# Optimization experiments

Hardware: AMD Instinct MI355X
Metric: run time of the kernel (lower is better)

## Reference

```python
import jax, jax.numpy as jnp
import numpy as np

EPS = 1e-5  # nn.LayerNorm default
TOP_K = 2


def setup_inputs() -> dict:
    key = jax.random.key(0)
    ks = jax.random.split(key, 8)
    B, S, D, H, E = 4, 2048, 512, 512, 8
    sd = lambda fan_in: 1.0 / np.sqrt(fan_in)
    x = jax.random.normal(ks[0], (B, S, D), dtype=jnp.float32)
    # gate: Linear(D, E, bias=False)
    Wg = jax.random.uniform(ks[1], (D, E), jnp.float32, -sd(D), sd(D))
    # stacked expert params (ExpertModule): fc1 D->H, fc2 H->D, LayerNorm(D)
    W1 = jax.random.uniform(ks[2], (E, D, H), jnp.float32, -sd(D), sd(D))
    b1 = jax.random.uniform(ks[3], (E, H), jnp.float32, -sd(D), sd(D))
    W2 = jax.random.uniform(ks[4], (E, H, D), jnp.float32, -sd(H), sd(H))
    b2 = jax.random.uniform(ks[5], (E, D), jnp.float32, -sd(H), sd(H))
    gamma = jnp.ones((E, D), jnp.float32)
    beta = jnp.zeros((E, D), jnp.float32)
    return {"x": x, "Wg": Wg, "W1": W1, "b1": b1, "W2": W2, "b2": b2,
            "gamma": gamma, "beta": beta}


def _moe_forward(x, Wg, W1, b1, W2, b2, gamma, beta):
    B, S, D = x.shape
    xf = x.reshape(-1, D)                                   # [T, D]
    # gating: top-k logits then softmax over the k selected logits only
    logits = xf @ Wg                                        # [T, E]
    topv, topi = jax.lax.top_k(logits, TOP_K)               # [T, K]
    gate_w = jax.nn.softmax(topv, axis=-1)                  # [T, K]
    # expert MLP + LayerNorm computed for all experts (dropout inactive in eval)
    h = jax.nn.relu(jnp.einsum('td,edh->teh', xf, W1) + b1[None])   # [T, E, H]
    y = jnp.einsum('teh,ehd->ted', h, W2) + b2[None]                 # [T, E, D]
    mu = jnp.mean(y, axis=-1, keepdims=True)
    var = jnp.mean((y - mu) ** 2, axis=-1, keepdims=True)
    y = (y - mu) / jnp.sqrt(var + EPS) * gamma[None] + beta[None]
    # combine: gather the k selected expert outputs and weight-sum
    y_sel = jnp.take_along_axis(y, topi[:, :, None], axis=1)        # [T, K, D]
    out = jnp.sum(gate_w[:, :, None] * y_sel, axis=1)               # [T, D]
    return out.reshape(B, S, D)


def reference(x, Wg, W1, b1, W2, b2, gamma, beta):
    return _moe_forward(x, Wg, W1, b1, W2, b2, gamma, beta)
```

## Files before the change

kernel.cpp:

```cpp
#include <hip/hip_runtime.h>
#include <hip/hip_bf16.h>


#define T_TOK   8192
#define DDIM    512
#define HDIM    512
#define NEXP    8
#define NASSIGN (T_TOK * 2)
#define CPAD    16
#define CAP     4096
#define MT      40

typedef _Float16 f16x8 __attribute__((ext_vector_type(8)));
typedef _Float16 f16x4 __attribute__((ext_vector_type(4)));
typedef float    f32x4 __attribute__((ext_vector_type(4)));

__device__ __forceinline__ void gld_lds16(const _Float16* g, _Float16* l) {
    __builtin_amdgcn_global_load_lds(
        (const __attribute__((address_space(1))) unsigned int*)g,
        (__attribute__((address_space(3))) unsigned int*)l,
        16, 0, 0);
}

__global__ __launch_bounds__(256) void prep_kernel(
    const float* __restrict__ x,
    const float* __restrict__ Wg,
    const float* __restrict__ W1,
    const float* __restrict__ W2,
    _Float16* __restrict__ xh,
    int* __restrict__ ei,
    float* __restrict__ gw,
    int* __restrict__ cursor,
    int* __restrict__ rowtok,
    int* __restrict__ pos,
    _Float16* __restrict__ W1t,
    _Float16* __restrict__ W2t)
{
    __shared__ float wgt[NEXP][512];
    __shared__ float tile[32][33];
    __shared__ int lcnt[NEXP];
    __shared__ int gbase[NEXP];

    int bid = blockIdx.x;
    int tid = threadIdx.x;

    if (bid < 2048) {
        if (tid < NEXP) lcnt[tid] = 0;
#pragma unroll
        for (int r = 0; r < 2; r++) {
            int d = r * 256 + tid;
            const float4* wr = (const float4*)(Wg + (size_t)d * NEXP);
            float4 a = wr[0], b = wr[1];
            wgt[0][d] = a.x; wgt[1][d] = a.y; wgt[2][d] = a.z; wgt[3][d] = a.w;
            wgt[4][d] = b.x; wgt[5][d] = b.y; wgt[6][d] = b.z; wgt[7][d] = b.w;
        }
        __syncthreads();

        int lane = tid & 63;
        int wave = tid >> 6;
        int t = bid * 4 + wave;

        double acc[NEXP];
#pragma unroll
        for (int e = 0; e < NEXP; e++) acc[e] = 0.0;

#pragma unroll
        for (int jj = 0; jj < 2; jj++) {
            int d0 = jj * 256 + lane * 4;
            float4 xv = *(const float4*)(x + (size_t)t * DDIM + d0);
            f16x4 hv;
            hv[0] = (_Float16)xv.x; hv[1] = (_Float16)xv.y;
            hv[2] = (_Float16)xv.z; hv[3] = (_Float16)xv.w;
            *(f16x4*)(xh + (size_t)t * DDIM + d0) = hv;
            double xd[4] = {(double)xv.x, (double)xv.y, (double)xv.z, (double)xv.w};
#pragma unroll
            for (int e = 0; e < NEXP; e++) {
                f32x4 wv = *(const f32x4*)(&wgt[e][d0]);
#pragma unroll
                for (int c = 0; c < 4; c++)
                    acc[e] += xd[c] * (double)wv[c];
            }
        }
#pragma unroll
        for (int off = 1; off < 8; off <<= 1) {
#pragma unroll
            for (int e = 0; e < NEXP; e++) acc[e] += __shfl_xor(acc[e], off, 64);
        }
        double v = acc[0];
#pragma unroll
        for (int e = 1; e < NEXP; e++) if ((lane & 7) == e) v = acc[e];
#pragma unroll
        for (int off = 8; off < 64; off <<= 1) v += __shfl_xor(v, off, 64);
        double lv[NEXP];
#pragma unroll
        for (int e = 0; e < NEXP; e++) lv[e] = __shfl(v, e, 64);

        double v0 = -1e300; int i0 = 0;
#pragma unroll
        for (int e = 0; e < NEXP; e++) if (lv[e] > v0) { v0 = lv[e]; i0 = e; }
        double v1 = -1e300; int i1 = (i0 == 0) ? 1 : 0;
#pragma unroll
        for (int e = 0; e < NEXP; e++) if (e != i0 && lv[e] > v1) { v1 = lv[e]; i1 = e; }

        int lr0 = 0, lr1 = 0;
        if (lane == 0) {
            double ex = exp(v1 - v0);
            float g0 = (float)(1.0 / (1.0 + ex));
            float g1 = (float)(ex / (1.0 + ex));
            ei[2 * t] = i0;  ei[2 * t + 1] = i1;
            gw[2 * t] = g0;  gw[2 * t + 1] = g1;
            lr0 = atomicAdd(&lcnt[i0], 1);
            lr1 = atomicAdd(&lcnt[i1], 1);
        }
        __syncthreads();
        if (tid < NEXP) {
            int c = lcnt[tid];
            gbase[tid] = c ? atomicAdd(&cursor[tid * CPAD], c) : 0;
        }
        __syncthreads();
        if (lane == 0) {
            int r0 = i0 * CAP + gbase[i0] + lr0;
            int r1 = i1 * CAP + gbase[i1] + lr1;
            rowtok[r0] = 2 * t;      pos[2 * t] = r0;
            rowtok[r1] = 2 * t + 1;  pos[2 * t + 1] = r1;
        }
    } else {
        int b2 = bid - 2048;
        int z = b2 >> 8;
        int rem = b2 & 255;
        int by = (rem >> 4) * 32;
        int bx = (rem & 15) * 32;
        const float* src;
        _Float16* dst;
        if (z < 8) { src = W1 + (size_t)z * 512 * 512; dst = W1t + (size_t)z * 512 * 512; }
        else       { src = W2 + (size_t)(z - 8) * 512 * 512; dst = W2t + (size_t)(z - 8) * 512 * 512; }
        int tx = tid & 31, ty = tid >> 5;
#pragma unroll
        for (int i = 0; i < 4; i++) {
            int r = by + ty + i * 8;
            tile[ty + i * 8][tx] = src[(size_t)r * 512 + bx + tx];
        }
        __syncthreads();
        int row = tid >> 3;
        int jc  = tid & 7;
        f16x4 v;
#pragma unroll
        for (int k = 0; k < 4; k++) v[k] = (_Float16)tile[jc * 4 + k][row];
        *(f16x4*)(dst + (size_t)(bx + row) * 512 + by + jc * 4) = v;
    }
}

template <bool GATHER, bool RELU>
__global__ __launch_bounds__(256) void gemm_tile(
    const _Float16* __restrict__ A,
    const _Float16* __restrict__ Bt,
    const float* __restrict__ bias,
    const int* __restrict__ rowtok,
    const int* __restrict__ cursor,
    _Float16* __restrict__ C)
{
    int bid = blockIdx.x;
    int e = bid & 7;
    int j = bid >> 3;
    int ne = cursor[e * CPAD];
    int m0 = (j >> 2) * 64;
    if (m0 >= ne) return;
    int n0 = (j & 3) * 128;
    int off = e * CAP;
    const _Float16* Bte = Bt + (size_t)e * 512 * 512;

    __shared__ _Float16 As[2][64 * 32];
    __shared__ _Float16 Bs[2][128 * 32];

    int tid = threadIdx.x;
    int lane = tid & 63;
    int wave = tid >> 6;
    int wm = (wave >> 1) * 32;
    int wn = (wave & 1) * 64;
    int quad = lane >> 4;
    int l16 = lane & 15;

    int srow = tid >> 2;
    int ksw = ((tid & 3) ^ ((srow >> 1) & 3)) * 8;

    int rg0 = m0 + srow;
    int cr0 = off + (rg0 < ne ? rg0 : ne - 1);
    const _Float16* arow;
    if (GATHER) arow = A + (size_t)(rowtok[cr0] >> 1) * 512;
    else        arow = A + (size_t)cr0 * 512;
    const _Float16* brow0 = Bte + (size_t)(n0 + srow) * 512;
    const _Float16* brow1 = Bte + (size_t)(n0 + srow + 64) * 512;

    f32x4 acc[2][4];
#pragma unroll
    for (int i = 0; i < 2; i++)
#pragma unroll
        for (int jj = 0; jj < 4; jj++) {
            acc[i][jj][0] = 0.f; acc[i][jj][1] = 0.f;
            acc[i][jj][2] = 0.f; acc[i][jj][3] = 0.f;
        }

    int rsw = (quad ^ ((l16 >> 1) & 3)) * 8;

    gld_lds16(arow + ksw, &As[0][tid * 8]);
    gld_lds16(brow0 + ksw, &Bs[0][tid * 8]);
    gld_lds16(brow1 + ksw, &Bs[0][tid * 8 + 64 * 32]);
    __syncthreads();

    int cur = 0;
    for (int t = 0; t < 16; ++t) {
        if (t < 15) {
            int k1 = (t + 1) * 32;
            gld_lds16(arow + k1 + ksw, &As[cur ^ 1][tid * 8]);
            gld_lds16(brow0 + k1 + ksw, &Bs[cur ^ 1][tid * 8]);
            gld_lds16(brow1 + k1 + ksw, &Bs[cur ^ 1][tid * 8 + 64 * 32]);
        }

        f16x8 af[2], bf[4];
#pragma unroll
        for (int i = 0; i < 2; i++)
            af[i] = *(const f16x8*)(&As[cur][(wm + i * 16 + l16) * 32 + rsw]);
#pragma unroll
        for (int jj = 0; jj < 4; jj++)
            bf[jj] = *(const f16x8*)(&Bs[cur][(wn + jj * 16 + l16) * 32 + rsw]);
#pragma unroll
        for (int i = 0; i < 2; i++)
#pragma unroll
            for (int jj = 0; jj < 4; jj++)
                acc[i][jj] = __builtin_amdgcn_mfma_f32_16x16x32_f16(af[i], bf[jj], acc[i][jj], 0, 0, 0);

        if (t < 15) {
            __syncthreads();
            cur ^= 1;
        }
    }

    float bcol[4];
#pragma unroll
    for (int jj = 0; jj < 4; jj++) bcol[jj] = bias[(size_t)e * 512 + n0 + wn + jj * 16 + l16];
#pragma unroll
    for (int i = 0; i < 2; i++) {
#pragma unroll
        for (int rr = 0; rr < 4; rr++) {
            int rg = m0 + wm + i * 16 + quad * 4 + rr;
            if (rg < ne) {
#pragma unroll
                for (int jj = 0; jj < 4; jj++) {
                    float v = acc[i][jj][rr] + bcol[jj];
                    if (RELU) v = fmaxf(v, 0.0f);
                    C[(size_t)(off + rg) * 512 + n0 + wn + jj * 16 + l16] = (_Float16)v;
                }
            }
        }
    }
}

__global__ void ln_combine_kernel(const _Float16* __restrict__ yb,
                                  const int* __restrict__ pos,
                                  const float* __restrict__ gw,
                                  const int* __restrict__ ei,
                                  const float* __restrict__ gamma,
                                  const float* __restrict__ beta,
                                  float* __restrict__ out) {
    int t = blockIdx.x * 4 + (threadIdx.x >> 6);
    int lane = threadIdx.x & 63;
    float o[8];
#pragma unroll
    for (int j = 0; j < 8; j++) o[j] = 0.0f;

#pragma unroll
    for (int k = 0; k < 2; k++) {
        int s = 2 * t + k;
        int r = pos[s];
        int e = ei[s];
        float w = gw[s];
        f16x8 v = *(const f16x8*)(yb + (size_t)r * 512 + lane * 8);
        float f[8];
        float sum = 0.f, sq = 0.f;
#pragma unroll
        for (int j = 0; j < 8; j++) { f[j] = (float)v[j]; sum += f[j]; sq += f[j] * f[j]; }
#pragma unroll
        for (int off = 1; off < 64; off <<= 1) {
            sum += __shfl_xor(sum, off, 64);
            sq  += __shfl_xor(sq, off, 64);
        }
        float mu = sum * (1.0f / 512.0f);
        float var = sq * (1.0f / 512.0f) - mu * mu;
        float rstd = rsqrtf(var + 1e-5f);
#pragma unroll
        for (int j = 0; j < 8; j++) {
            int d = lane * 8 + j;
            o[j] += w * ((f[j] - mu) * rstd * gamma[(size_t)e * 512 + d] + beta[(size_t)e * 512 + d]);
        }
    }
    float4* op = (float4*)(out + (size_t)t * 512 + lane * 8);
    op[0] = make_float4(o[0], o[1], o[2], o[3]);
    op[1] = make_float4(o[4], o[5], o[6], o[7]);
}

extern "C" void kernel_launch(void* const* d_in, const int* in_sizes, int n_in,
                              void* d_out, int out_size, void* d_ws, size_t ws_size,
                              hipStream_t stream) {
    const float* x     = (const float*)d_in[0];
    const float* Wg    = (const float*)d_in[1];
    const float* W1    = (const float*)d_in[2];
    const float* b1    = (const float*)d_in[3];
    const float* W2    = (const float*)d_in[4];
    const float* b2    = (const float*)d_in[5];
    const float* gamma = (const float*)d_in[6];
    const float* beta  = (const float*)d_in[7];
    float* out = (float*)d_out;

    char* w = (char*)d_ws;
    size_t o = 0;
    auto alloc = [&](size_t bytes) -> void* {
        void* p = w + o;
        o += (bytes + 255) & ~(size_t)255;
        return p;
    };
    _Float16* xh  = (_Float16*)alloc((size_t)T_TOK * DDIM * 2);
    _Float16* W1t = (_Float16*)alloc((size_t)NEXP * DDIM * HDIM * 2);
    _Float16* W2t = (_Float16*)alloc((size_t)NEXP * DDIM * HDIM * 2);
    _Float16* hb  = (_Float16*)alloc((size_t)NEXP * CAP * HDIM * 2);
    _Float16* yb  = (_Float16*)alloc((size_t)NEXP * CAP * DDIM * 2);
    float* gw     = (float*)alloc((size_t)NASSIGN * 4);
    int* ei       = (int*)alloc((size_t)NASSIGN * 4);
    int* rowtok   = (int*)alloc((size_t)NEXP * CAP * 4);
    int* pos      = (int*)alloc((size_t)NASSIGN * 4);
    int* cursor   = (int*)alloc(NEXP * CPAD * 4);
    (void)ws_size; (void)n_in; (void)in_sizes; (void)out_size;

    hipMemsetAsync(cursor, 0, NEXP * CPAD * sizeof(int), stream);

    prep_kernel<<<6144, 256, 0, stream>>>(x, Wg, W1, W2, xh, ei, gw,
                                          cursor, rowtok, pos, W1t, W2t);

    gemm_tile<true, true><<<1280, 256, 0, stream>>>(xh, W1t, b1, rowtok, cursor, hb);
    gemm_tile<false, false><<<1280, 256, 0, stream>>>(hb, W2t, b2, nullptr, cursor, yb);

    ln_combine_kernel<<<2048, 256, 0, stream>>>(yb, pos, gw, ei, gamma, beta, out);
}
```

Before: 167.5 us.

## Enlarge prep blocks to 1024 threads, ballot-based expert slot allocation, vectorize combine loads

The prep kernel now uses 1024-thread blocks that handle 16 tokens (or four transpose tiles) each, which cuts the number of blocks and the redundant per-block loads of the gate weights. Slot allocation moves from shared-memory atomics plus two barriers to one wave doing ballot/popcount grouping with a single global atomic per expert. The x loads are issued before the gate-weight staging so they overlap. The combine kernel loads pos/ei/gw as vector pairs and gamma/beta as float4. Larger blocks may lower occupancy flexibility, and rows are now assigned within an expert in a different order.

```diff
diff --git a/kernel.cpp b/kernel.cpp
--- a/kernel.cpp
+++ b/kernel.cpp
@@ -22,7 +22,7 @@
         16, 0, 0);
 }
 
-__global__ __launch_bounds__(256) void prep_kernel(
+__global__ __launch_bounds__(1024) void prep_kernel(
     const float* __restrict__ x,
     const float* __restrict__ Wg,
     const float* __restrict__ W1,
@@ -36,42 +36,51 @@
     _Float16* __restrict__ W1t,
     _Float16* __restrict__ W2t)
 {
-    __shared__ float wgt[NEXP][512];
-    __shared__ float tile[32][33];
-    __shared__ int lcnt[NEXP];
-    __shared__ int gbase[NEXP];
+    __shared__ float smf[4 * 32 * 33];
+    __shared__ int earr[32];
 
     int bid = blockIdx.x;
     int tid = threadIdx.x;
 
-    if (bid < 2048) {
-        if (tid < NEXP) lcnt[tid] = 0;
-#pragma unroll
-        for (int r = 0; r < 2; r++) {
-            int d = r * 256 + tid;
-            const float4* wr = (const float4*)(Wg + (size_t)d * NEXP);
-            float4 a = wr[0], b = wr[1];
-            wgt[0][d] = a.x; wgt[1][d] = a.y; wgt[2][d] = a.z; wgt[3][d] = a.w;
-            wgt[4][d] = b.x; wgt[5][d] = b.y; wgt[6][d] = b.z; wgt[7][d] = b.w;
-        }
-        __syncthreads();
-
+    if (bid < 512) {
+        float (*wgt)[512] = (float (*)[512])smf;
         int lane = tid & 63;
         int wave = tid >> 6;
-        int t = bid * 4 + wave;
+        int t = bid * 16 + wave;
+
+        const float* xr = x + (size_t)t * DDIM;
+        float4 xv0 = *(const float4*)(xr + lane * 4);
+        float4 xv1 = *(const float4*)(xr + 256 + lane * 4);
+
+        if (tid < 256) {
+#pragma unroll
+            for (int r = 0; r < 2; r++) {
+                int d = r * 256 + tid;
+                const float4* wr = (const float4*)(Wg + (size_t)d * NEXP);
+                float4 a = wr[0], b = wr[1];
+                wgt[0][d] = a.x; wgt[1][d] = a.y; wgt[2][d] = a.z; wgt[3][d] = a.w;
+                wgt[4][d] = b.x; wgt[5][d] = b.y; wgt[6][d] = b.z; wgt[7][d] = b.w;
+            }
+        }
+
+        {
+            f16x4 h0, h1;
+            h0[0] = (_Float16)xv0.x; h0[1] = (_Float16)xv0.y;
+            h0[2] = (_Float16)xv0.z; h0[3] = (_Float16)xv0.w;
+            h1[0] = (_Float16)xv1.x; h1[1] = (_Float16)xv1.y;
+            h1[2] = (_Float16)xv1.z; h1[3] = (_Float16)xv1.w;
+            *(f16x4*)(xh + (size_t)t * DDIM + lane * 4) = h0;
+            *(f16x4*)(xh + (size_t)t * DDIM + 256 + lane * 4) = h1;
+        }
+        __syncthreads();
 
         double acc[NEXP];
 #pragma unroll
         for (int e = 0; e < NEXP; e++) acc[e] = 0.0;
-
 #pragma unroll
         for (int jj = 0; jj < 2; jj++) {
+            float4 xv = jj ? xv1 : xv0;
             int d0 = jj * 256 + lane * 4;
-            float4 xv = *(const float4*)(x + (size_t)t * DDIM + d0);
-            f16x4 hv;
-            hv[0] = (_Float16)xv.x; hv[1] = (_Float16)xv.y;
-            hv[2] = (_Float16)xv.z; hv[3] = (_Float16)xv.w;
-            *(f16x4*)(xh + (size_t)t * DDIM + d0) = hv;
             double xd[4] = {(double)xv.x, (double)xv.y, (double)xv.z, (double)xv.w};
 #pragma unroll
             for (int e = 0; e < NEXP; e++) {
@@ -102,30 +111,44 @@
 #pragma unroll
         for (int e = 0; e < NEXP; e++) if (e != i0 && lv[e] > v1) { v1 = lv[e]; i1 = e; }
 
-        int lr0 = 0, lr1 = 0;
         if (lane == 0) {
             double ex = exp(v1 - v0);
             float g0 = (float)(1.0 / (1.0 + ex));
             float g1 = (float)(ex / (1.0 + ex));
             ei[2 * t] = i0;  ei[2 * t + 1] = i1;
             gw[2 * t] = g0;  gw[2 * t + 1] = g1;
-            lr0 = atomicAdd(&lcnt[i0], 1);
-            lr1 = atomicAdd(&lcnt[i1], 1);
+            earr[wave * 2] = i0;
+            earr[wave * 2 + 1] = i1;
         }
         __syncthreads();
-        if (tid < NEXP) {
-            int c = lcnt[tid];
-            gbase[tid] = c ? atomicAdd(&cursor[tid * CPAD], c) : 0;
-        }
-        __syncthreads();
-        if (lane == 0) {
-            int r0 = i0 * CAP + gbase[i0] + lr0;
-            int r1 = i1 * CAP + gbase[i1] + lr1;
-            rowtok[r0] = 2 * t;      pos[2 * t] = r0;
-            rowtok[r1] = 2 * t + 1;  pos[2 * t + 1] = r1;
+
+        if (wave == 0) {
+            int e = (lane < 32) ? earr[lane] : -1;
+            int r = 0;
+#pragma unroll
+            for (int ex = 0; ex < NEXP; ex++) {
+                unsigned long long mask = __ballot(e == ex);
+                if (e == ex) {
+                    int leader = __ffsll(mask) - 1;
+                    int cnt = __popcll(mask);
+                    unsigned long long below = mask & ((1ull << lane) - 1ull);
+                    int base = 0;
+                    if (lane == leader) base = atomicAdd(&cursor[ex * CPAD], cnt);
+                    base = __shfl(base, leader, 64);
+                    r = ex * CAP + base + __popcll(below);
+                }
+            }
+            if (lane < 32) {
+                int s = bid * 32 + lane;
+                rowtok[r] = s;
+                pos[s] = r;
+            }
         }
     } else {
-        int b2 = bid - 2048;
+        float (*tile)[32][33] = (float (*)[32][33])smf;
+        int sub = tid >> 8;
+        int stid = tid & 255;
+        int b2 = (bid - 512) * 4 + sub;
         int z = b2 >> 8;
         int rem = b2 & 255;
         int by = (rem >> 4) * 32;
@@ -134,18 +157,18 @@
         _Float16* dst;
         if (z < 8) { src = W1 + (size_t)z * 512 * 512; dst = W1t + (size_t)z * 512 * 512; }
         else       { src = W2 + (size_t)(z - 8) * 512 * 512; dst = W2t + (size_t)(z - 8) * 512 * 512; }
-        int tx = tid & 31, ty = tid >> 5;
+        int tx = stid & 31, ty = stid >> 5;
 #pragma unroll
         for (int i = 0; i < 4; i++) {
             int r = by + ty + i * 8;
-            tile[ty + i * 8][tx] = src[(size_t)r * 512 + bx + tx];
+            tile[sub][ty + i * 8][tx] = src[(size_t)r * 512 + bx + tx];
         }
         __syncthreads();
-        int row = tid >> 3;
-        int jc  = tid & 7;
+        int row = stid >> 3;
+        int jc  = stid & 7;
         f16x4 v;
 #pragma unroll
-        for (int k = 0; k < 4; k++) v[k] = (_Float16)tile[jc * 4 + k][row];
+        for (int k = 0; k < 4; k++) v[k] = (_Float16)tile[sub][jc * 4 + k][row];
         *(f16x4*)(dst + (size_t)(bx + row) * 512 + by + jc * 4) = v;
     }
 }
@@ -268,13 +291,22 @@
 #pragma unroll
     for (int j = 0; j < 8; j++) o[j] = 0.0f;
 
+    int2 pr = *(const int2*)(pos + 2 * t);
+    int2 er = *(const int2*)(ei + 2 * t);
+    float2 gr = *(const float2*)(gw + 2 * t);
+
 #pragma unroll
     for (int k = 0; k < 2; k++) {
-        int s = 2 * t + k;
-        int r = pos[s];
-        int e = ei[s];
-        float w = gw[s];
+        int r = k ? pr.y : pr.x;
+        int e = k ? er.y : er.x;
+        float w = k ? gr.y : gr.x;
         f16x8 v = *(const f16x8*)(yb + (size_t)r * 512 + lane * 8);
+        const float4* gp = (const float4*)(gamma + (size_t)e * 512 + lane * 8);
+        const float4* bp = (const float4*)(beta + (size_t)e * 512 + lane * 8);
+        float4 ga = gp[0], gb = gp[1];
+        float4 ba = bp[0], bb = bp[1];
+        float gvv[8] = {ga.x, ga.y, ga.z, ga.w, gb.x, gb.y, gb.z, gb.w};
+        float bvv[8] = {ba.x, ba.y, ba.z, ba.w, bb.x, bb.y, bb.z, bb.w};
         float f[8];
         float sum = 0.f, sq = 0.f;
 #pragma unroll
@@ -288,10 +320,8 @@
         float var = sq * (1.0f / 512.0f) - mu * mu;
         float rstd = rsqrtf(var + 1e-5f);
 #pragma unroll
-        for (int j = 0; j < 8; j++) {
-            int d = lane * 8 + j;
-            o[j] += w * ((f[j] - mu) * rstd * gamma[(size_t)e * 512 + d] + beta[(size_t)e * 512 + d]);
-        }
+        for (int j = 0; j < 8; j++)
+            o[j] += w * ((f[j] - mu) * rstd * gvv[j] + bvv[j]);
     }
     float4* op = (float4*)(out + (size_t)t * 512 + lane * 8);
     op[0] = make_float4(o[0], o[1], o[2], o[3]);
@@ -332,8 +362,8 @@
 
     hipMemsetAsync(cursor, 0, NEXP * CPAD * sizeof(int), stream);
 
-    prep_kernel<<<6144, 256, 0, stream>>>(x, Wg, W1, W2, xh, ei, gw,
-                                          cursor, rowtok, pos, W1t, W2t);
+    prep_kernel<<<1536, 1024, 0, stream>>>(x, Wg, W1, W2, xh, ei, gw,
+                                           cursor, rowtok, pos, W1t, W2t);
 
     gemm_tile<true, true><<<1280, 256, 0, stream>>>(xh, W1t, b1, rowtok, cursor, hb);
     gemm_tile<false, false><<<1280, 256, 0, stream>>>(hb, W2t, b2, nullptr, cursor, yb);
```

New measurement: 148.1 us. 11.6% less time.
